# Performance work log

Hardware: AMD Instinct MI355X
Metric: run time of the kernel (lower is better)

The kernel has to match this reference:

```python
import jax, jax.numpy as jnp
import numpy as np

N_NODES = 100000
N_EDGES = 625000
IN_DIM = 128
NUM_CLASSES = 2


def setup_inputs() -> dict:
    key = jax.random.key(0)
    k1, k2, k3 = jax.random.split(key, 3)
    x = jax.random.normal(k1, (N_NODES, IN_DIM), dtype=jnp.float32)
    edge_index = jax.random.randint(k2, (2, N_EDGES), 0, N_NODES, dtype=jnp.int64)
    # nn.Linear(2*in_dim, num_classes): weight [out, in], bias [out]
    W = jax.random.normal(k3, (NUM_CLASSES, 2 * IN_DIM), dtype=jnp.float32) * (1.0 / np.sqrt(2 * IN_DIM))
    b = jnp.zeros((NUM_CLASSES,), dtype=jnp.float32)
    return {"x": x, "edge_index": edge_index, "W": W, "b": b}


def reference(x, edge_index, W, b):
    # Gather src/dst node features per edge, concat, linear classifier.
    src, dst = edge_index[0], edge_index[1]
    h = jnp.concatenate([x[src], x[dst]], axis=-1)  # [E, 2*in_dim]
    score = jnp.einsum('ed,cd->ec', h, W) + b        # [E, num_classes]
    return score
```

## Files before the change

### kernel.cpp

```cpp
#include <hip/hip_runtime.h>
#include <hip/hip_bf16.h>

#define IN_DIM 128
#define NUM_CLASSES 2

__global__ __launch_bounds__(256) void node_proj_kernel(
    const float* __restrict__ x,
    const float* __restrict__ W,
    float4* __restrict__ p,
    int n_nodes) {
    const int lane = threadIdx.x & 63;
    const int gwave = (blockIdx.x * blockDim.x + threadIdx.x) >> 6;
    const int nwaves = (gridDim.x * blockDim.x) >> 6;

    const int dd = 2 * lane;
    const float2 wa0 = *(const float2*)(W + 0 * 256 + dd);
    const float2 wa1 = *(const float2*)(W + 1 * 256 + dd);
    const float2 wd0 = *(const float2*)(W + 0 * 256 + 128 + dd);
    const float2 wd1 = *(const float2*)(W + 1 * 256 + 128 + dd);

    for (int n = gwave; n < n_nodes; n += nwaves) {
        const float2 xv = *(const float2*)(x + (size_t)n * IN_DIM + dd);
        float a0 = xv.x * wa0.x + xv.y * wa0.y;
        float a1 = xv.x * wa1.x + xv.y * wa1.y;
        float d0 = xv.x * wd0.x + xv.y * wd0.y;
        float d1 = xv.x * wd1.x + xv.y * wd1.y;
        #pragma unroll
        for (int off = 32; off > 0; off >>= 1) {
            a0 += __shfl_xor(a0, off, 64);
            a1 += __shfl_xor(a1, off, 64);
            d0 += __shfl_xor(d0, off, 64);
            d1 += __shfl_xor(d1, off, 64);
        }
        if (lane == 0) {
            p[n] = make_float4(a0, a1, d0, d1);
        }
    }
}

__global__ __launch_bounds__(256) void edge_score_kernel(
    const int* __restrict__ idx,
    const float4* __restrict__ p,
    const float* __restrict__ b,
    float2* __restrict__ out,
    int n_edges) {
    const int e = blockIdx.x * blockDim.x + threadIdx.x;
    if (e >= n_edges) return;
    const int s = idx[e];
    const int d = idx[n_edges + e];
    const float4 ps = p[s];
    const float4 pd = p[d];
    const float b0 = b[0];
    const float b1 = b[1];
    float2 o;
    o.x = ps.x + pd.z + b0;
    o.y = ps.y + pd.w + b1;
    out[e] = o;
}

extern "C" void kernel_launch(void* const* d_in, const int* in_sizes, int n_in,
                              void* d_out, int out_size, void* d_ws, size_t ws_size,
                              hipStream_t stream) {
    const float* x   = (const float*)d_in[0];
    const int*   idx = (const int*)d_in[1];
    const float* W   = (const float*)d_in[2];
    const float* b   = (const float*)d_in[3];
    float* out = (float*)d_out;

    const int n_nodes = in_sizes[0] / IN_DIM;
    const int n_edges = in_sizes[1] / 2;

    float4* p = (float4*)d_ws;

    node_proj_kernel<<<1024, 256, 0, stream>>>(x, W, p, n_nodes);

    const int blocks = (n_edges + 255) / 256;
    edge_score_kernel<<<blocks, 256, 0, stream>>>(idx, p, b, (float2*)out, n_edges);
}
```

Baseline: 119.5 us.

## Restructure node projection to 4 lanes per node with LDS-staged weights

The node projection kernel now assigns 16 nodes per wave, with 4 lanes per node each covering 32 features. Each lane issues float4 loads of x and reads weights from a padded shared-memory copy, so the six-step 64-lane shuffle reduction per node shrinks to two shuffle steps. The grid-stride loop over 1024 blocks is replaced by one block per 64 nodes, so all memory requests are issued at once. The cost is a per-block LDS weight fill plus a barrier, and per-lane strided x accesses that may coalesce worse.

```diff
diff --git a/kernel.cpp b/kernel.cpp
--- a/kernel.cpp
+++ b/kernel.cpp
@@ -2,38 +2,60 @@
 #include <hip/hip_bf16.h>
 
 #define IN_DIM 128
-#define NUM_CLASSES 2
 
 __global__ __launch_bounds__(256) void node_proj_kernel(
     const float* __restrict__ x,
     const float* __restrict__ W,
     float4* __restrict__ p,
     int n_nodes) {
+    __shared__ __align__(16) float wlds[4 * 144];
+
+    for (int i = threadIdx.x; i < 512; i += 256) {
+        int c    = i >> 8;
+        int d    = i & 255;
+        int half = d >> 7;
+        int k    = d & 127;
+        int sub  = k >> 5;
+        int kk   = k & 31;
+        wlds[(half * 2 + c) * 144 + sub * 36 + kk] = W[i];
+    }
+    __syncthreads();
+
     const int lane = threadIdx.x & 63;
-    const int gwave = (blockIdx.x * blockDim.x + threadIdx.x) >> 6;
-    const int nwaves = (gridDim.x * blockDim.x) >> 6;
+    const int sub  = lane & 3;
+    const int nl   = lane >> 2;
+    const int wave = threadIdx.x >> 6;
+    const int node = (blockIdx.x * 4 + wave) * 16 + nl;
 
-    const int dd = 2 * lane;
-    const float2 wa0 = *(const float2*)(W + 0 * 256 + dd);
-    const float2 wa1 = *(const float2*)(W + 1 * 256 + dd);
-    const float2 wd0 = *(const float2*)(W + 0 * 256 + 128 + dd);
-    const float2 wd1 = *(const float2*)(W + 1 * 256 + 128 + dd);
+    if (node < n_nodes) {
+        const float* xb = x + (size_t)node * IN_DIM + sub * 32;
+        const float* wt = wlds + sub * 36;
 
-    for (int n = gwave; n < n_nodes; n += nwaves) {
-        const float2 xv = *(const float2*)(x + (size_t)n * IN_DIM + dd);
-        float a0 = xv.x * wa0.x + xv.y * wa0.y;
-        float a1 = xv.x * wa1.x + xv.y * wa1.y;
-        float d0 = xv.x * wd0.x + xv.y * wd0.y;
-        float d1 = xv.x * wd1.x + xv.y * wd1.y;
+        float a0 = 0.f, a1 = 0.f, d0 = 0.f, d1 = 0.f;
         #pragma unroll
-        for (int off = 32; off > 0; off >>= 1) {
-            a0 += __shfl_xor(a0, off, 64);
-            a1 += __shfl_xor(a1, off, 64);
-            d0 += __shfl_xor(d0, off, 64);
-            d1 += __shfl_xor(d1, off, 64);
+        for (int j = 0; j < 8; ++j) {
+            const float4 xv = *(const float4*)(xb + j * 4);
+            const float4 w0 = *(const float4*)(wt + 0 * 144 + j * 4);
+            const float4 w1 = *(const float4*)(wt + 1 * 144 + j * 4);
+            const float4 w2 = *(const float4*)(wt + 2 * 144 + j * 4);
+            const float4 w3 = *(const float4*)(wt + 3 * 144 + j * 4);
+            a0 += xv.x * w0.x + xv.y * w0.y + xv.z * w0.z + xv.w * w0.w;
+            a1 += xv.x * w1.x + xv.y * w1.y + xv.z * w1.z + xv.w * w1.w;
+            d0 += xv.x * w2.x + xv.y * w2.y + xv.z * w2.z + xv.w * w2.w;
+            d1 += xv.x * w3.x + xv.y * w3.y + xv.z * w3.z + xv.w * w3.w;
         }
-        if (lane == 0) {
-            p[n] = make_float4(a0, a1, d0, d1);
+
+        a0 += __shfl_xor(a0, 1, 64);
+        a1 += __shfl_xor(a1, 1, 64);
+        d0 += __shfl_xor(d0, 1, 64);
+        d1 += __shfl_xor(d1, 1, 64);
+        a0 += __shfl_xor(a0, 2, 64);
+        a1 += __shfl_xor(a1, 2, 64);
+        d0 += __shfl_xor(d0, 2, 64);
+        d1 += __shfl_xor(d1, 2, 64);
+
+        if (sub == 0) {
+            p[node] = make_float4(a0, a1, d0, d1);
         }
     }
 }
@@ -72,8 +94,9 @@
 
     float4* p = (float4*)d_ws;
 
-    node_proj_kernel<<<1024, 256, 0, stream>>>(x, W, p, n_nodes);
+    const int blocks1 = (n_nodes + 63) / 64;
+    node_proj_kernel<<<blocks1, 256, 0, stream>>>(x, W, p, n_nodes);
 
-    const int blocks = (n_edges + 255) / 256;
-    edge_score_kernel<<<blocks, 256, 0, stream>>>(idx, p, b, (float2*)out, n_edges);
+    const int blocks2 = (n_edges + 255) / 256;
+    edge_score_kernel<<<blocks2, 256, 0, stream>>>(idx, p, b, (float2*)out, n_edges);
 }
```

Result: faster. 101.2 us (-15.3%).
